# Kernel tuning notes

Measured on AMD Instinct MI355X. Metric: run time of the kernel, lower is better.

Reference implementation:

```python
import jax, jax.numpy as jnp
import numpy as np

B, M, L = 100, 100, 8
N = M * L
EPS = 1e-5  # torch BatchNorm2d default eps


def _conv(x, w, b, stride, pad):
    y = jax.lax.conv_general_dilated(x, w, (stride, stride), [(pad, pad), (pad, pad)],
                                     dimension_numbers=('NCHW', 'OIHW', 'NCHW'))
    return y + b[None, :, None, None]


def _convT(x, w, b, stride, pad):
    # torch ConvTranspose2d weight layout: (in_ch, out_ch, kH, kW)
    k = w.shape[2]
    wt = jnp.flip(w, (2, 3)).transpose(1, 0, 2, 3)  # -> OIHW
    p = k - 1 - pad
    y = jax.lax.conv_general_dilated(x, wt, (1, 1), [(p, p), (p, p)],
                                     lhs_dilation=(stride, stride),
                                     dimension_numbers=('NCHW', 'OIHW', 'NCHW'))
    return y + b[None, :, None, None]


def _bn(x):
    # BatchNorm2d constructed fresh in forward: weight=1, bias=0, batch stats (biased var)
    mean = x.mean(axis=(0, 2, 3), keepdims=True)
    var = x.var(axis=(0, 2, 3), keepdims=True)
    return (x - mean) / jnp.sqrt(var + EPS)


def _leaky(x):
    return jnp.where(x >= 0, x, 0.01 * x)


def _forward(x, conv1_w, conv1_b, conv2_w, conv2_b, conv3_w, conv3_b, conv4_w, conv4_b,
             fc_w, fc_b, dec_w, dec_b, ct1_w, ct1_b, ct2_w, ct2_b, ct3_w, ct3_b,
             ct4_w, ct4_b, ct5_w, ct5_b):
    # ---- encoder ----
    h = _bn(_leaky(_conv(x, conv1_w, conv1_b, 2, 1)))   # (B,128,32,32)
    h = _bn(_leaky(_conv(h, conv2_w, conv2_b, 2, 1)))   # (B,256,16,16)
    h = _bn(_leaky(_conv(h, conv3_w, conv3_b, 2, 1)))   # (B,1024,8,8)
    h = _bn(_leaky(_conv(h, conv4_w, conv4_b, 2, 1)))   # (B,1024,4,4)
    eig = jax.nn.relu(h.reshape(B, -1) @ fc_w + fc_b)   # (B, 800)
    # ---- latent_sample (training branch) ----
    sig = eig.reshape(B, M, L)
    row = jnp.sqrt(float(M * L)) * jnp.fft.ifft2(sig)          # complex (B,M,L)
    # original builds C via numpy/scipy per-sample -> detached; circulant[i,j] = c[(i-j) % n]
    row_flat = jax.lax.stop_gradient(row.real.reshape(B, N))
    i = jnp.arange(N)
    idx = (i[:, None] - i[None, :]) % N                        # (N,N) circulant gather
    C = row_flat[:, idx]                                       # (B,N,N)
    # original: Sigma_batch_eps[:, i] = eigenvalue (noise zeta is dead code), via numpy -> detached
    Y = jnp.fft.fft2(jax.lax.stop_gradient(sig)).real          # (B,M,L)
    # ---- decoder ----
    d = (Y.reshape(B, N) @ dec_w + dec_b).reshape(B, 1024, 3, 3)
    d = _convT(d, ct1_w, ct1_b, 2, 1)   # (B,512,5,5)
    d = _convT(d, ct2_w, ct2_b, 2, 0)   # (B,256,11,11)
    d = _convT(d, ct3_w, ct3_b, 2, 0)   # (B,128,23,23)
    d = _convT(d, ct4_w, ct4_b, 2, 0)   # (B,64,47,47)
    d = _convT(d, ct5_w, ct5_b, 1, 0)   # (B,1,49,49)
    return d, C, eig


def setup_inputs():
    key = jax.random.key(0)
    ks = jax.random.split(key, 16)

    def wv(k, shape, fan_in):
        return (jax.random.normal(k, shape, jnp.float32) / np.sqrt(fan_in)).astype(jnp.float32)

    return {
        'x': jax.random.normal(ks[0], (B, 1, 64, 64), jnp.float32),
        'conv1_w': wv(ks[1], (128, 1, 3, 3), 9), 'conv1_b': jnp.zeros((128,), jnp.float32),
        'conv2_w': wv(ks[2], (256, 128, 3, 3), 128 * 9), 'conv2_b': jnp.zeros((256,), jnp.float32),
        'conv3_w': wv(ks[3], (1024, 256, 3, 3), 256 * 9), 'conv3_b': jnp.zeros((1024,), jnp.float32),
        'conv4_w': wv(ks[4], (1024, 1024, 3, 3), 1024 * 9), 'conv4_b': jnp.zeros((1024,), jnp.float32),
        'fc_w': wv(ks[5], (1024 * 16, N), 1024 * 16), 'fc_b': jnp.zeros((N,), jnp.float32),
        'dec_w': wv(ks[6], (N, 1024 * 9), N), 'dec_b': jnp.zeros((1024 * 9,), jnp.float32),
        'ct1_w': wv(ks[7], (1024, 512, 3, 3), 1024 * 9), 'ct1_b': jnp.zeros((512,), jnp.float32),
        'ct2_w': wv(ks[8], (512, 256, 3, 3), 512 * 9), 'ct2_b': jnp.zeros((256,), jnp.float32),
        'ct3_w': wv(ks[9], (256, 128, 3, 3), 256 * 9), 'ct3_b': jnp.zeros((128,), jnp.float32),
        'ct4_w': wv(ks[10], (128, 64, 3, 3), 128 * 9), 'ct4_b': jnp.zeros((64,), jnp.float32),
        'ct5_w': wv(ks[11], (64, 1, 3, 3), 64 * 9), 'ct5_b': jnp.zeros((1,), jnp.float32),
    }


def reference(x, conv1_w, conv1_b, conv2_w, conv2_b, conv3_w, conv3_b, conv4_w, conv4_b,
              fc_w, fc_b, dec_w, dec_b, ct1_w, ct1_b, ct2_w, ct2_b, ct3_w, ct3_b,
              ct4_w, ct4_b, ct5_w, ct5_b):
    return _forward(x, conv1_w, conv1_b, conv2_w, conv2_b, conv3_w, conv3_b, conv4_w, conv4_b,
                    fc_w, fc_b, dec_w, dec_b, ct1_w, ct1_b, ct2_w, ct2_b, ct3_w, ct3_b,
                    ct4_w, ct4_b, ct5_w, ct5_b)
```

## Files before the change

### kernel.cpp

```cpp
#include <hip/hip_runtime.h>
#include <math.h>

typedef __attribute__((ext_vector_type(8))) short bf16x8;
typedef __attribute__((ext_vector_type(4))) float f32x4;
typedef unsigned short u16;

__device__ __forceinline__ u16 f2bf(float f) {
    unsigned u = __builtin_bit_cast(unsigned, f);
    u += 0x7FFFu + ((u >> 16) & 1u);
    return (u16)(u >> 16);
}
__device__ __forceinline__ float bf2f(u16 h) {
    unsigned u = ((unsigned)h) << 16;
    return __builtin_bit_cast(float, u);
}

template<int MODE, int OUT, int BM, int BN, int SWIZ, bool STATS>
__global__ __launch_bounds__(256, 3)
void gemm(const u16* __restrict__ Abf, const u16* __restrict__ Bw,
          const float* __restrict__ bias, void* __restrict__ outv,
          float* __restrict__ stat,
          int M, int N, int K, int lgC,
          int IH, int IW, int OH, int OW, int zchunk)
{
    constexpr int ANSEG = BM / 64, BNSEG = BN / 64;
    constexpr int RM = BM / 32, RN = BN / 32;
    __shared__ __align__(16) u16 As[2][4 * BM * 8];
    __shared__ __align__(16) u16 Bs[2][4 * BN * 8];
    const int t = threadIdx.x;
    const int lane = t & 63, wave = t >> 6;
    const int lm = lane & 15, quad = lane >> 4;
    const int wm = wave & 1, wn = wave >> 1;
    int mt, nt, z;
    if (SWIZ == 1) {
        int mtN = (M + BM - 1) / BM;
        int id = blockIdx.x;
        nt = id & 7; int j = id >> 3;
        mt = j % mtN; z = j / mtN;
    } else { mt = blockIdx.x; nt = blockIdx.y; z = blockIdx.z; }
    const int k0 = z * zchunk, kend = k0 + zchunk;

    const int arow = (ANSEG == 2) ? (t >> 1) : (t >> 2);
    const int akb  = (ANSEG == 2) ? (t & 1) * 16 : (t & 3) * 8;
    const int a_gm = mt * BM + arow;
    const bool a_in = a_gm < M;
    int oy = 0, ox = 0, bimg = 0;
    if (MODE == 1) {
        int ohw = OH * OW;
        int g = a_in ? a_gm : 0;
        bimg = g / ohw; int r = g - bimg * ohw;
        oy = r / OW; ox = r - (r / OW) * OW;
    }
    const int brow = (BNSEG == 2) ? (t >> 1) : (t >> 2);
    const int bkb  = (BNSEG == 2) ? (t & 1) * 16 : (t & 3) * 8;
    const int b_gn = nt * BN + brow;
    const bool b_in = b_gn < N;

    const int Cmask = (1 << lgC) - 1;
    int ic_s = 0, tap_s = 0;
    bool aok = a_in;
    const u16* aptr;
    if (MODE == 0) {
        aptr = Abf + (size_t)a_gm * K + k0 + akb;
    } else {
        int kk0 = k0 + akb;
        tap_s = kk0 >> lgC; ic_s = kk0 & Cmask;
        int ky = tap_s / 3, kx = tap_s - (tap_s / 3) * 3;
        int iy = oy * 2 - 1 + ky, ix = ox * 2 - 1 + kx;
        aok = a_in && (unsigned)iy < (unsigned)IH && (unsigned)ix < (unsigned)IW;
        aptr = Abf + ((((size_t)bimg * IH + iy) * IW + ix) << lgC);
    }
    const u16* bptr = Bw + (size_t)b_gn * K + k0 + bkb;

    auto ldA = [&](uint4 (&v)[ANSEG]) {
        #pragma unroll
        for (int s = 0; s < ANSEG; s++) {
            uint4 x4 = make_uint4(0, 0, 0, 0);
            if (MODE == 0) {
                if (aok) x4 = *(const uint4*)(aptr + s * 8);
            } else {
                if (aok) x4 = *(const uint4*)(aptr + ic_s + s * 8);
            }
            v[s] = x4;
        }
        if (MODE == 0) {
            aptr += 32;
        } else {
            ic_s += 32;
            if (ic_s > Cmask) {
                ic_s -= Cmask + 1;
                tap_s++;
                int ky = tap_s / 3, kx = tap_s - (tap_s / 3) * 3;
                int iy = oy * 2 - 1 + ky, ix = ox * 2 - 1 + kx;
                aok = a_in && (unsigned)iy < (unsigned)IH && (unsigned)ix < (unsigned)IW;
                aptr = Abf + ((((size_t)bimg * IH + iy) * IW + ix) << lgC);
            }
        }
    };
    auto ldB = [&](uint4 (&v)[BNSEG]) {
        #pragma unroll
        for (int s = 0; s < BNSEG; s++) {
            uint4 x4 = make_uint4(0, 0, 0, 0);
            if (b_in) x4 = *(const uint4*)(bptr + s * 8);
            v[s] = x4;
        }
        bptr += 32;
    };

    f32x4 acc[RM][RN];
    #pragma unroll
    for (int i = 0; i < RM; i++)
        #pragma unroll
        for (int j = 0; j < RN; j++) acc[i][j] = (f32x4){0.f, 0.f, 0.f, 0.f};

    uint4 va[ANSEG], vb[BNSEG];
    ldA(va); ldB(vb);
    int buf = 0;
    for (int kb = k0; kb < kend; kb += 32) {
        #pragma unroll
        for (int s = 0; s < ANSEG; s++)
            *(uint4*)&As[buf][(((akb >> 3) + s) * BM + arow) * 8] = va[s];
        #pragma unroll
        for (int s = 0; s < BNSEG; s++)
            *(uint4*)&Bs[buf][(((bkb >> 3) + s) * BN + brow) * 8] = vb[s];
        __syncthreads();
        if (kb + 32 < kend) { ldA(va); ldB(vb); }
        bf16x8 af[RM], bfr[RN];
        #pragma unroll
        for (int i = 0; i < RM; i++)
            af[i] = *(const bf16x8*)&As[buf][(size_t)(quad * BM + wm * (BM / 2) + i * 16 + lm) * 8];
        #pragma unroll
        for (int j = 0; j < RN; j++)
            bfr[j] = *(const bf16x8*)&Bs[buf][(size_t)(quad * BN + wn * (BN / 2) + j * 16 + lm) * 8];
        #pragma unroll
        for (int i = 0; i < RM; i++)
            #pragma unroll
            for (int j = 0; j < RN; j++)
                acc[i][j] = __builtin_amdgcn_mfma_f32_16x16x32_bf16(af[i], bfr[j], acc[i][j], 0, 0, 0);
        buf ^= 1;
    }

    const int n_base = nt * BN + wn * (BN / 2);
    const int m_base = mt * BM + wm * (BM / 2);
    int nj[RN]; float bvj[RN];
    #pragma unroll
    for (int j = 0; j < RN; j++) {
        nj[j] = n_base + j * 16 + lm;
        bvj[j] = 0.f;
        if (nj[j] < N && OUT != 4) {
            if (OUT == 0) bvj[j] = bias[nj[j]];
            else if (OUT == 6) bvj[j] = bias[(nj[j] & 1023) * 9 + (nj[j] >> 10)];
            else if (z == 0) bvj[j] = bias[nj[j]];
        }
    }
    if constexpr (OUT == 4) {
        float* op = (float*)outv;
        #pragma unroll
        for (int i = 0; i < RM; i++)
            #pragma unroll
            for (int r = 0; r < 4; r++) {
                int m = m_base + i * 16 + quad * 4 + r;
                if (m >= M) continue;
                #pragma unroll
                for (int j = 0; j < RN; j++)
                    if (nj[j] < N) atomicAdd(&op[(size_t)m * N + nj[j]], acc[i][j][r]);
            }
    } else if constexpr (OUT == 6) {
        u16* op = (u16*)outv;
        #pragma unroll
        for (int i = 0; i < RM; i++)
            #pragma unroll
            for (int r = 0; r < 4; r++) {
                int m = m_base + i * 16 + quad * 4 + r;
                if (m >= M) continue;
                #pragma unroll
                for (int j = 0; j < RN; j++)
                    if (nj[j] < N) op[(size_t)m * N + nj[j]] = f2bf(acc[i][j][r] + bvj[j]);
            }
    } else if constexpr (OUT == 0) {
        int ohw = OH * OW;
        float sj[RN], qj[RN];
        #pragma unroll
        for (int j = 0; j < RN; j++) { sj[j] = 0.f; qj[j] = 0.f; }
        #pragma unroll
        for (int i = 0; i < RM; i++) {
            int m0 = m_base + i * 16 + quad * 4;
            if (m0 >= M) continue;
            int b = m0 / ohw, pix = m0 - b * ohw;
            #pragma unroll
            for (int j = 0; j < RN; j++) {
                if (nj[j] >= N) continue;
                #pragma unroll
                for (int r = 0; r < 4; r++) {
                    float val = acc[i][j][r] + bvj[j];
                    ((u16*)outv)[((size_t)b * ohw + pix + r) * N + nj[j]] = f2bf(val);
                    if (STATS) {
                        float lv = val >= 0.f ? val : 0.01f * val;
                        sj[j] += lv; qj[j] += lv * lv;
                    }
                }
            }
        }
        if constexpr (STATS) {
            #pragma unroll
            for (int j = 0; j < RN; j++) {
                float s = sj[j], q = qj[j];
                s += __shfl_down(s, 32); q += __shfl_down(q, 32);
                s += __shfl_down(s, 16); q += __shfl_down(q, 16);
                if (quad == 0 && nj[j] < N) {
                    atomicAdd(&stat[nj[j]], s);
                    atomicAdd(&stat[N + nj[j]], q);
                }
            }
        }
    } else {
        int ohw = OH * OW;
        #pragma unroll
        for (int i = 0; i < RM; i++) {
            int m0 = m_base + i * 16 + quad * 4;
            if (m0 >= M) continue;
            int b = m0 / ohw, pix = m0 - b * ohw;
            #pragma unroll
            for (int j = 0; j < RN; j++) {
                if (nj[j] >= N) continue;
                #pragma unroll
                for (int r = 0; r < 4; r++)
                    atomicAdd(&((float*)outv)[((size_t)b * ohw + pix + r) * N + nj[j]],
                              acc[i][j][r] + bvj[j]);
            }
        }
    }
}

template<int BM>
__global__ __launch_bounds__(256, 3)
void gemm_ct(const u16* __restrict__ Abf, const u16* __restrict__ Wb,
             const float* __restrict__ bias, u16* __restrict__ out,
             int N, int lgC, int IH, int IW, int OH, int OW,
             int4 Kc, int4 Mc, int4 Hc, int4 Wc, int4 Oc, int4 Dy, int4 Dx)
{
    constexpr int ANSEG = BM / 64;
    constexpr int RM = BM / 32, RN = 2;
    const int c = blockIdx.z;
    const int Ks[4] = {Kc.x, Kc.y, Kc.z, Kc.w};
    const int Ms[4] = {Mc.x, Mc.y, Mc.z, Mc.w};
    const int Hs[4] = {Hc.x, Hc.y, Hc.z, Hc.w};
    const int Wsz[4]= {Wc.x, Wc.y, Wc.z, Wc.w};
    const int Os[4] = {Oc.x, Oc.y, Oc.z, Oc.w};
    const int Dys[4]= {Dy.x, Dy.y, Dy.z, Dy.w};
    const int Dxs[4]= {Dx.x, Dx.y, Dx.z, Dx.w};
    const int K = Ks[c], M = Ms[c], OHc = Hs[c], OWc = Wsz[c];
    const int dyp = Dys[c], dxp = Dxs[c];
    const int mt = blockIdx.x, nt = blockIdx.y;
    if (mt * BM >= M) return;
    const u16* Bw = Wb + Os[c];

    __shared__ __align__(16) u16 As[2][4 * BM * 8];
    __shared__ __align__(16) u16 Bs[2][4 * 64 * 8];
    const int t = threadIdx.x;
    const int lane = t & 63, wave = t >> 6;
    const int lm = lane & 15, quad = lane >> 4;
    const int wm = wave & 1, wn = wave >> 1;

    const int arow = (ANSEG == 2) ? (t >> 1) : (t >> 2);
    const int akb  = (ANSEG == 2) ? (t & 1) * 16 : (t & 3) * 8;
    const int a_gm = mt * BM + arow;
    const bool a_in = a_gm < M;
    const int ohwc = OHc * OWc;
    int g = a_in ? a_gm : 0;
    int bimg = g / ohwc; int rr = g - bimg * ohwc;
    int oy = rr / OWc, ox = rr - (rr / OWc) * OWc;

    const int brow = t >> 2;
    const int bkb  = (t & 3) * 8;
    const int b_gn = nt * 64 + brow;
    const bool b_in = b_gn < N;

    const int Cmask = (1 << lgC) - 1;
    int ic_s = akb & Cmask;
    int ti_s = 0;
    bool aok; const u16* aptr;
    {
        int sh = 8 * (ti_s & 3);
        int dy = (int)(signed char)((dyp >> sh) & 255);
        int dx = (int)(signed char)((dxp >> sh) & 255);
        int iy = oy + dy, ix = ox + dx;
        aok = a_in && (unsigned)iy < (unsigned)IH && (unsigned)ix < (unsigned)IW;
        aptr = Abf + ((((size_t)bimg * IH + iy) * IW + ix) << lgC);
    }
    const u16* bptr = Bw + (size_t)b_gn * K + bkb;

    auto ldA = [&](uint4 (&v)[ANSEG]) {
        #pragma unroll
        for (int s = 0; s < ANSEG; s++) {
            uint4 x4 = make_uint4(0, 0, 0, 0);
            if (aok) x4 = *(const uint4*)(aptr + ic_s + s * 8);
            v[s] = x4;
        }
        ic_s += 32;
        if (ic_s > Cmask) {
            ic_s -= Cmask + 1;
            ti_s++;
            int sh = 8 * (ti_s & 3);
            int dy = (int)(signed char)((dyp >> sh) & 255);
            int dx = (int)(signed char)((dxp >> sh) & 255);
            int iy = oy + dy, ix = ox + dx;
            aok = a_in && (unsigned)iy < (unsigned)IH && (unsigned)ix < (unsigned)IW;
            aptr = Abf + ((((size_t)bimg * IH + iy) * IW + ix) << lgC);
        }
    };
    auto ldB = [&](uint4& v) {
        uint4 x4 = make_uint4(0, 0, 0, 0);
        if (b_in) x4 = *(const uint4*)bptr;
        v = x4;
        bptr += 32;
    };

    f32x4 acc[RM][RN];
    #pragma unroll
    for (int i = 0; i < RM; i++)
        #pragma unroll
        for (int j = 0; j < RN; j++) acc[i][j] = (f32x4){0.f, 0.f, 0.f, 0.f};

    uint4 va[ANSEG]; uint4 vb;
    ldA(va); ldB(vb);
    int buf = 0;
    for (int kb = 0; kb < K; kb += 32) {
        #pragma unroll
        for (int s = 0; s < ANSEG; s++)
            *(uint4*)&As[buf][(((akb >> 3) + s) * BM + arow) * 8] = va[s];
        *(uint4*)&Bs[buf][((bkb >> 3) * 64 + brow) * 8] = vb;
        __syncthreads();
        if (kb + 32 < K) { ldA(va); ldB(vb); }
        bf16x8 af[RM], bfr[RN];
        #pragma unroll
        for (int i = 0; i < RM; i++)
            af[i] = *(const bf16x8*)&As[buf][(size_t)(quad * BM + wm * (BM / 2) + i * 16 + lm) * 8];
        #pragma unroll
        for (int j = 0; j < RN; j++)
            bfr[j] = *(const bf16x8*)&Bs[buf][(size_t)(quad * 64 + wn * 32 + j * 16 + lm) * 8];
        #pragma unroll
        for (int i = 0; i < RM; i++)
            #pragma unroll
            for (int j = 0; j < RN; j++)
                acc[i][j] = __builtin_amdgcn_mfma_f32_16x16x32_bf16(af[i], bfr[j], acc[i][j], 0, 0, 0);
        buf ^= 1;
    }

    const int n_base = nt * 64 + wn * 32;
    const int m_base = mt * BM + wm * (BM / 2);
    const int cy = c >> 1, cx = c & 1;
    const int OHW = OH * OW;
    int nj[RN]; float bvj[RN];
    #pragma unroll
    for (int j = 0; j < RN; j++) {
        nj[j] = n_base + j * 16 + lm;
        bvj[j] = (nj[j] < N) ? bias[nj[j]] : 0.f;
    }
    #pragma unroll
    for (int i = 0; i < RM; i++)
        #pragma unroll
        for (int r = 0; r < 4; r++) {
            int m = m_base + i * 16 + quad * 4 + r;
            if (m >= M) continue;
            int b = m / ohwc, r2 = m - b * ohwc;
            int oyc = r2 / OWc, oxc = r2 - (r2 / OWc) * OWc;
            size_t ad0 = ((size_t)b * OHW + (2 * oyc + cy) * OW + 2 * oxc + cx) * N;
            #pragma unroll
            for (int j = 0; j < RN; j++)
                if (nj[j] < N) out[ad0 + nj[j]] = f2bf(acc[i][j][r] + bvj[j]);
        }
}

__global__ __launch_bounds__(256)
void convw_prep(const float* __restrict__ src, u16* __restrict__ dst, int lgC) {
    __shared__ float tl[9216];
    int CIN = 1 << lgC;
    int n = CIN * 9;
    size_t base = (size_t)blockIdx.x * n;
    for (int i = threadIdx.x; i < n; i += 256) tl[i] = src[base + i];
    __syncthreads();
    for (int j = threadIdx.x; j < n; j += 256) {
        int tap = j >> lgC, ic = j & (CIN - 1);
        dst[base + j] = f2bf(tl[ic * 9 + tap]);
    }
}

__global__ __launch_bounds__(256)
void transpose_cvt_dec(const float* __restrict__ in, u16* __restrict__ out) {
    __shared__ float tl[32][33];
    int c0 = blockIdx.x * 32, r0 = blockIdx.y * 32;
    int tx = threadIdx.x & 31, ty = threadIdx.x >> 5;
    #pragma unroll
    for (int l = 0; l < 4; l++)
        tl[ty + 8 * l][tx] = in[(size_t)(r0 + ty + 8 * l) * 9216 + c0 + tx];
    __syncthreads();
    #pragma unroll
    for (int l = 0; l < 4; l++) {
        int n = c0 + ty + 8 * l;
        int cc = n / 9, hw = n - 9 * cc;
        out[(size_t)(hw * 1024 + cc) * 800 + r0 + tx] = f2bf(tl[tx][ty + 8 * l]);
    }
}

__global__ __launch_bounds__(256)
void ctw_fused(const float* __restrict__ in, u16* __restrict__ outw,
               int CIN, int P, int4 Kc, int4 Oc) {
    __shared__ float tl[32][33];
    int c0 = blockIdx.x * 32, r0 = blockIdx.y * 32;
    int C = gridDim.x * 32;
    int tx = threadIdx.x & 31, ty = threadIdx.x >> 5;
    #pragma unroll
    for (int l = 0; l < 4; l++)
        tl[ty + 8 * l][tx] = in[(size_t)(r0 + ty + 8 * l) * C + c0 + tx];
    __syncthreads();
    const int Ks[4] = {Kc.x, Kc.y, Kc.z, Kc.w};
    const int Os[4] = {Oc.x, Oc.y, Oc.z, Oc.w};
    int ic = r0 + tx;
    #pragma unroll
    for (int l = 0; l < 4; l++) {
        int cc = c0 + ty + 8 * l;
        int oc = cc / 9, tap = cc - 9 * oc;
        int ky = tap / 3, kx = tap - 3 * (tap / 3);
        int cyc = (P + ky) & 1, cxc = (P + kx) & 1;
        int cls = cyc * 2 + cxc;
        int nkx = ((P ^ cxc) & 1) ? 1 : 2;
        int ti = (ky >> 1) * nkx + (kx >> 1);
        outw[Os[cls] + (size_t)oc * Ks[cls] + ti * CIN + ic] = f2bf(tl[tx][ty + 8 * l]);
    }
}

__global__ __launch_bounds__(256)
void fcw_prep(const float* __restrict__ in, u16* __restrict__ out) {
    __shared__ float tl[32][33];
    int n0 = blockIdx.x * 32, c0 = blockIdx.y * 32, hw = blockIdx.z;
    int tx = threadIdx.x & 31, ty = threadIdx.x >> 5;
    #pragma unroll
    for (int l = 0; l < 4; l++)
        tl[ty + 8 * l][tx] = in[((size_t)(c0 + ty + 8 * l) * 16 + hw) * 800 + n0 + tx];
    __syncthreads();
    #pragma unroll
    for (int l = 0; l < 4; l++)
        out[(size_t)(n0 + ty + 8 * l) * 16384 + hw * 1024 + c0 + tx] = f2bf(tl[tx][ty + 8 * l]);
}

__global__ __launch_bounds__(256)
void wt5_prep(const float* __restrict__ in, u16* __restrict__ out) {
    int idx = blockIdx.x * 256 + threadIdx.x;
    if (idx >= 576) return;
    int tap = idx >> 6, ic = idx & 63;
    out[idx] = f2bf(in[ic * 9 + tap]);
}

__global__ __launch_bounds__(256)
void conv1_stat(const float* __restrict__ x, const float* __restrict__ w,
                const float* __restrict__ bias, u16* __restrict__ out,
                float* __restrict__ accum) {
    __shared__ float ls[256];
    ls[threadIdx.x] = 0.f;
    __syncthreads();
    int idx0 = blockIdx.x * 256 + threadIdx.x;
    int oc = idx0 & 127;
    float wreg[9];
    const float* wp = w + oc * 9;
    #pragma unroll
    for (int k = 0; k < 9; k++) wreg[k] = wp[k];
    float bz = bias[oc];
    float s = 0.f, q = 0.f;
    for (int idx = idx0; idx < 13107200; idx += 262144) {
        int pix = (idx >> 7) & 1023;
        int b = idx >> 17;
        int oy = pix >> 5, ox = pix & 31;
        int iy0 = oy * 2 - 1, ix0 = ox * 2 - 1;
        float acc = bz;
        const float* ip = x + (size_t)b * 4096;
        #pragma unroll
        for (int ky = 0; ky < 3; ky++) {
            int iy = iy0 + ky;
            if ((unsigned)iy >= 64u) continue;
            #pragma unroll
            for (int kx = 0; kx < 3; kx++) {
                int ix = ix0 + kx;
                if ((unsigned)ix >= 64u) continue;
                acc = fmaf(ip[iy * 64 + ix], wreg[ky * 3 + kx], acc);
            }
        }
        out[idx] = f2bf(acc);
        float lv = acc >= 0.f ? acc : 0.01f * acc;
        s += lv; q += lv * lv;
    }
    atomicAdd(&ls[oc], s);
    atomicAdd(&ls[128 + oc], q);
    __syncthreads();
    atomicAdd(&accum[threadIdx.x], ls[threadIdx.x]);
}

__global__ __launch_bounds__(256)
void bnapply8(const u16* __restrict__ x, u16* __restrict__ out,
              const float* __restrict__ accum, int C, int total, float invcnt) {
    int i8 = (blockIdx.x * 256 + threadIdx.x) * 8;
    if (i8 >= total) return;
    int c0 = i8 & (C - 1);
    uint4 v = *(const uint4*)(x + i8);
    const unsigned* w = (const unsigned*)&v;
    uint4 o;
    unsigned* ow = (unsigned*)&o;
    #pragma unroll
    for (int h = 0; h < 4; h++) {
        float m0 = accum[c0 + 2 * h] * invcnt, m1 = accum[c0 + 2 * h + 1] * invcnt;
        float q0 = accum[C + c0 + 2 * h] * invcnt, q1 = accum[C + c0 + 2 * h + 1] * invcnt;
        float in0 = rsqrtf(q0 - m0 * m0 + 1e-5f);
        float in1 = rsqrtf(q1 - m1 * m1 + 1e-5f);
        float v0 = __builtin_bit_cast(float, w[h] << 16);
        float v1 = __builtin_bit_cast(float, w[h] & 0xFFFF0000u);
        v0 = v0 >= 0.f ? v0 : 0.01f * v0;
        v1 = v1 >= 0.f ? v1 : 0.01f * v1;
        unsigned r0 = f2bf((v0 - m0) * in0);
        unsigned r1 = f2bf((v1 - m1) * in1);
        ow[h] = r0 | (r1 << 16);
    }
    *(uint4*)(out + i8) = o;
}

__global__ __launch_bounds__(256)
void bnstat4f(const float* __restrict__ x, float* __restrict__ accum, int C, int total) {
    __shared__ float ls[2048];
    for (int i = threadIdx.x; i < 2 * C; i += 256) ls[i] = 0.f;
    __syncthreads();
    int base = (blockIdx.x * 256 + threadIdx.x) * 4;
    int stride = gridDim.x * 1024;
    float s[4] = {0, 0, 0, 0}, q[4] = {0, 0, 0, 0};
    for (int i = base; i < total; i += stride) {
        f32x4 v = *(const f32x4*)(x + i);
        #pragma unroll
        for (int r = 0; r < 4; r++) {
            float vv = v[r]; vv = vv >= 0.f ? vv : 0.01f * vv;
            s[r] += vv; q[r] += vv * vv;
        }
    }
    int c0 = base & (C - 1);
    #pragma unroll
    for (int r = 0; r < 4; r++) {
        atomicAdd(&ls[c0 + r], s[r]);
        atomicAdd(&ls[C + c0 + r], q[r]);
    }
    __syncthreads();
    for (int i = threadIdx.x; i < 2 * C; i += 256) atomicAdd(&accum[i], ls[i]);
}

__global__ __launch_bounds__(256)
void bnapply4f(const float* __restrict__ x, u16* __restrict__ out,
               const float* __restrict__ accum, int C, int total, float invcnt) {
    int i4 = (blockIdx.x * 256 + threadIdx.x) * 4;
    if (i4 >= total) return;
    int c0 = i4 & (C - 1);
    f32x4 v = *(const f32x4*)(x + i4);
    unsigned r4[4];
    #pragma unroll
    for (int r = 0; r < 4; r++) {
        float m = accum[c0 + r] * invcnt;
        float var = accum[C + c0 + r] * invcnt - m * m;
        float inv = rsqrtf(var + 1e-5f);
        float vv = v[r]; vv = vv >= 0.f ? vv : 0.01f * vv;
        r4[r] = f2bf((vv - m) * inv);
    }
    *(uint2*)(out + i4) = make_uint2(r4[0] | (r4[1] << 16), r4[2] | (r4[3] << 16));
}

__global__ __launch_bounds__(256)
void dft_real(const float* __restrict__ facc, const float* __restrict__ fcb,
              float* __restrict__ eig, float* __restrict__ Yr, u16* __restrict__ Yrb) {
    __shared__ float se[800];
    __shared__ float ctab[800];
    int b = blockIdx.x;
    for (int i = threadIdx.x; i < 800; i += 256) {
        float v = fmaxf(facc[b * 800 + i] + fcb[i], 0.f);
        se[i] = v;
        if (blockIdx.y == 0) eig[b * 800 + i] = v;
        ctab[i] = cospif(i * 0.0025f);
    }
    __syncthreads();
    int o0 = blockIdx.y * 400;
    for (int oi = o0 + threadIdx.x; oi < o0 + 400; oi += 256) {
        int k1 = oi >> 3, k2 = oi & 7;
        int d1 = k1 * 8, d2 = k2 * 100;
        float acc0 = 0.f, acc1 = 0.f;
        int p1 = 0;
        for (int n1 = 0; n1 < 100; n1 += 2) {
            int p = p1;
            #pragma unroll
            for (int n2 = 0; n2 < 8; n2++) {
                acc0 = fmaf(se[n1 * 8 + n2], ctab[p], acc0);
                p += d2; if (p >= 800) p -= 800;
            }
            int pb = p1 + d1; if (pb >= 800) pb -= 800;
            int p2 = pb;
            #pragma unroll
            for (int n2 = 0; n2 < 8; n2++) {
                acc1 = fmaf(se[(n1 + 1) * 8 + n2], ctab[p2], acc1);
                p2 += d2; if (p2 >= 800) p2 -= 800;
            }
            p1 = pb + d1; if (p1 >= 800) p1 -= 800;
        }
        float acc = acc0 + acc1;
        Yr[b * 800 + oi] = acc;
        Yrb[b * 800 + oi] = f2bf(acc);
    }
}

__global__ __launch_bounds__(256)
void build_C4(const float* __restrict__ Yr, float* __restrict__ C) {
    int idx = blockIdx.x * 256 + threadIdx.x;
    if (idx >= 100 * 800 * 200) return;
    int j4 = (idx % 200) * 4; int tt = idx / 200;
    int i = tt % 800;         int b = tt / 800;
    const float* y = Yr + b * 800;
    f32x4 v;
    #pragma unroll
    for (int r = 0; r < 4; r++) {
        int k = i - (j4 + r);
        k += (k >> 31) & 800;
        v[r] = y[k] * 0.035355339059327376f;
    }
    ((f32x4*)C)[idx] = v;
}

__global__ __launch_bounds__(256)
void convT5(const u16* __restrict__ in, const u16* __restrict__ w,
            const float* __restrict__ bias, float* __restrict__ out) {
    int idx = blockIdx.x * 256 + threadIdx.x;
    if (idx >= 100 * 49 * 49) return;
    int ox = idx % 49; int t2 = idx / 49;
    int oy = t2 % 49;  int b = t2 / 49;
    float ac[8];
    #pragma unroll
    for (int r = 0; r < 8; r++) ac[r] = 0.f;
    for (int ky = 0; ky < 3; ky++) {
        int iy = oy - ky;
        if ((unsigned)iy >= 47u) continue;
        for (int kx = 0; kx < 3; kx++) {
            int ix = ox - kx;
            if ((unsigned)ix >= 47u) continue;
            const uint4* ip = (const uint4*)(in + (((size_t)b * 47 + iy) * 47 + ix) * 64);
            const uint4* wp = (const uint4*)(w + (ky * 3 + kx) * 64);
            #pragma unroll
            for (int g = 0; g < 8; g++) {
                uint4 av = ip[g], wv = wp[g];
                const unsigned* aa = (const unsigned*)&av;
                const unsigned* ww = (const unsigned*)&wv;
                #pragma unroll
                for (int h = 0; h < 4; h++) {
                    float a0 = __builtin_bit_cast(float, aa[h] << 16);
                    float a1 = __builtin_bit_cast(float, aa[h] & 0xFFFF0000u);
                    float w0 = __builtin_bit_cast(float, ww[h] << 16);
                    float w1 = __builtin_bit_cast(float, ww[h] & 0xFFFF0000u);
                    int rix = ((g & 1) << 2) | h;
                    ac[rix] = fmaf(a0, w0, ac[rix]);
                    ac[rix] = fmaf(a1, w1, ac[rix]);
                }
            }
        }
    }
    out[idx] = bias[0] + ((ac[0] + ac[1]) + (ac[2] + ac[3]))
                       + ((ac[4] + ac[5]) + (ac[6] + ac[7]));
}

struct CTClass { int T, OHc, OWc, dyp, dxp, off, K; };
static void ct_params(int P, int OH, int OW, int CIN, int OC, CTClass cls[4]) {
    int off = 0;
    for (int c = 0; c < 4; c++) {
        int cy = c >> 1, cx = c & 1;
        int kys[2], dys[2], nky = 0, kxs[2], dxs[2], nkx = 0;
        for (int ky = 0; ky < 3; ky++)
            if (((cy + P + ky) & 1) == 0) { kys[nky] = ky; dys[nky] = (cy + P - ky) / 2; nky++; }
        for (int kx = 0; kx < 3; kx++)
            if (((cx + P + kx) & 1) == 0) { kxs[nkx] = kx; dxs[nkx] = (cx + P - kx) / 2; nkx++; }
        CTClass& cc = cls[c];
        cc.T = nky * nkx;
        cc.OHc = (OH - cy + 1) >> 1; cc.OWc = (OW - cx + 1) >> 1;
        cc.dyp = 0; cc.dxp = 0;
        int ti = 0;
        for (int a = 0; a < nky; a++)
            for (int b2 = 0; b2 < nkx; b2++, ti++) {
                cc.dyp |= (dys[a] & 255) << (8 * ti);
                cc.dxp |= (dxs[b2] & 255) << (8 * ti);
            }
        cc.off = off; cc.K = CIN * cc.T;
        off += OC * cc.K;
    }
}

template<int BM>
static void launch_ct(hipStream_t s, const u16* in, const u16* W, const float* bias, u16* outp,
                      int lgC, int OC, int IH, int IW, int OH, int OW, const CTClass* cls) {
    int maxMT = 0;
    for (int c = 0; c < 4; c++) {
        int mt = (100 * cls[c].OHc * cls[c].OWc + BM - 1) / BM;
        if (mt > maxMT) maxMT = mt;
    }
    dim3 g(maxMT, (OC + 63) / 64, 4);
    gemm_ct<BM><<<g, 256, 0, s>>>(in, W, bias, outp, OC, lgC, IH, IW, OH, OW,
        make_int4(cls[0].K, cls[1].K, cls[2].K, cls[3].K),
        make_int4(100*cls[0].OHc*cls[0].OWc, 100*cls[1].OHc*cls[1].OWc,
                  100*cls[2].OHc*cls[2].OWc, 100*cls[3].OHc*cls[3].OWc),
        make_int4(cls[0].OHc, cls[1].OHc, cls[2].OHc, cls[3].OHc),
        make_int4(cls[0].OWc, cls[1].OWc, cls[2].OWc, cls[3].OWc),
        make_int4(cls[0].off, cls[1].off, cls[2].off, cls[3].off),
        make_int4(cls[0].dyp, cls[1].dyp, cls[2].dyp, cls[3].dyp),
        make_int4(cls[0].dxp, cls[1].dxp, cls[2].dxp, cls[3].dxp));
}

static void launch_ctw(hipStream_t s, const float* w, u16* outw,
                       int CIN, int OC, int P, const CTClass* cls) {
    dim3 g((OC * 9) / 32, CIN / 32);
    ctw_fused<<<g, 256, 0, s>>>(w, outw, CIN, P,
        make_int4(cls[0].K, cls[1].K, cls[2].K, cls[3].K),
        make_int4(cls[0].off, cls[1].off, cls[2].off, cls[3].off));
}

extern "C" void kernel_launch(void* const* d_in, const int* in_sizes, int n_in,
                              void* d_out, int out_size, void* d_ws, size_t ws_size,
                              hipStream_t stream) {
    const float* x    = (const float*)d_in[0];
    const float* c1w  = (const float*)d_in[1];  const float* c1b = (const float*)d_in[2];
    const float* c2w  = (const float*)d_in[3];  const float* c2b = (const float*)d_in[4];
    const float* c3w  = (const float*)d_in[5];  const float* c3b = (const float*)d_in[6];
    const float* c4w  = (const float*)d_in[7];  const float* c4b = (const float*)d_in[8];
    const float* fcw  = (const float*)d_in[9];  const float* fcb = (const float*)d_in[10];
    const float* decw = (const float*)d_in[11]; const float* decb = (const float*)d_in[12];
    const float* t1w  = (const float*)d_in[13]; const float* t1b = (const float*)d_in[14];
    const float* t2w  = (const float*)d_in[15]; const float* t2b = (const float*)d_in[16];
    const float* t3w  = (const float*)d_in[17]; const float* t3b = (const float*)d_in[18];
    const float* t4w  = (const float*)d_in[19]; const float* t4b = (const float*)d_in[20];
    const float* t5w  = (const float*)d_in[21]; const float* t5b = (const float*)d_in[22];

    float* out = (float*)d_out;
    float* d_final = out;
    float* Cmat    = out + 240100;
    float* eig     = out + 240100 + 64000000;

    float* ws = (float*)d_ws;
    u16*   h1    = (u16*)(ws);
    u16*   W_fc  = (u16*)(ws);
    u16*   h2    = (u16*)(ws + 6553600);
    u16*   h3    = (u16*)(ws + 9830400);
    u16*   W_c2  = (u16*)(ws + 13107200);
    u16*   W_c3  = (u16*)(ws + 13254656);
    u16*   W_c4  = (u16*)(ws + 14434304);
    float* h4f   = ws + 19152896;
    u16*   h4    = (u16*)(ws + 20791296);
    float* accs  = ws + 21610496;
    float* facc  = ws + 21618688;
    float* Yr    = ws + 21698688;
    u16*   Yrb   = (u16*)(ws + 21778688);
    u16*   d0    = (u16*)(ws + 21818688);
    u16*   W_dec = (u16*)(ws + 22279488);
    float* acc1 = accs, *acc2 = accs + 2048, *acc3 = accs + 4096, *acc4 = accs + 6144;
    u16*   W_t   = (u16*)(ws);
    u16*   o1    = (u16*)(ws + 4718592);
    u16*   o2    = (u16*)(ws + 5358592);
    u16*   o3    = (u16*)(ws + 6907392);
    u16*   o4    = (u16*)(ws + 10292992);
    u16*   W_t5  = (u16*)(ws + 17361792);

    #define GRID(n) dim3(((n) + 255) / 256)

    hipMemsetAsync(accs, 0, (8192 + 80000) * 4, stream);

    conv1_stat<<<dim3(1024), 256, 0, stream>>>(x, c1w, c1b, h1, acc1);
    bnapply8<<<GRID(1638400), 256, 0, stream>>>(h1, h1, acc1, 128, 13107200, 1.f / 102400.f);

    convw_prep<<<dim3(256), 256, 0, stream>>>(c2w, W_c2, 7);
    gemm<1, 0, 128, 128, 0, true><<<dim3(200, 2, 1), 256, 0, stream>>>(
        h1, W_c2, c2b, h2, acc2, 25600, 256, 1152, 7, 32, 32, 16, 16, 1152);
    bnapply8<<<GRID(819200), 256, 0, stream>>>(h2, h2, acc2, 256, 6553600, 1.f / 25600.f);

    convw_prep<<<dim3(1024), 256, 0, stream>>>(c3w, W_c3, 8);
    gemm<1, 0, 128, 128, 1, true><<<dim3(400, 1, 1), 256, 0, stream>>>(
        h2, W_c3, c3b, h3, acc3, 6400, 1024, 2304, 8, 16, 16, 8, 8, 2304);
    bnapply8<<<GRID(819200), 256, 0, stream>>>(h3, h3, acc3, 1024, 6553600, 1.f / 6400.f);

    convw_prep<<<dim3(1024), 256, 0, stream>>>(c4w, W_c4, 10);
    hipMemsetAsync(h4f, 0, 1638400 * 4, stream);
    gemm<1, 1, 64, 128, 1, false><<<dim3(400, 1, 1), 256, 0, stream>>>(
        h3, W_c4, c4b, h4f, nullptr, 1600, 1024, 9216, 10, 8, 8, 4, 4, 4608);
    bnstat4f<<<1024, 256, 0, stream>>>(h4f, acc4, 1024, 1638400);
    bnapply4f<<<GRID(409600), 256, 0, stream>>>(h4f, h4, acc4, 1024, 1638400, 1.f / 1600.f);

    fcw_prep<<<dim3(25, 32, 16), 256, 0, stream>>>(fcw, W_fc);
    gemm<0, 4, 64, 64, 0, false><<<dim3(2, 13, 16), 256, 0, stream>>>(
        h4, W_fc, nullptr, facc, nullptr, 100, 800, 16384, 0, 0, 0, 0, 0, 1024);

    dft_real<<<dim3(100, 2), 256, 0, stream>>>(facc, fcb, eig, Yr, Yrb);
    build_C4<<<GRID(16000000), 256, 0, stream>>>(Yr, Cmat);

    transpose_cvt_dec<<<dim3(288, 25), 256, 0, stream>>>(decw, W_dec);
    gemm<0, 6, 64, 64, 0, false><<<dim3(2, 144, 1), 256, 0, stream>>>(
        Yrb, W_dec, decb, d0, nullptr, 100, 9216, 800, 0, 0, 0, 0, 0, 800);

    CTClass c1c[4], c2c[4], c3c[4], c4c[4];
    ct_params(1, 5, 5, 1024, 512, c1c);
    ct_params(0, 11, 11, 512, 256, c2c);
    ct_params(0, 23, 23, 256, 128, c3c);
    ct_params(0, 47, 47, 128, 64, c4c);

    launch_ctw(stream, t1w, W_t, 1024, 512, 1, c1c);
    launch_ct<64>(stream, d0, W_t, t1b, o1, 10, 512, 3, 3, 5, 5, c1c);

    launch_ctw(stream, t2w, W_t, 512, 256, 0, c2c);
    launch_ct<64>(stream, o1, W_t, t2b, o2, 9, 256, 5, 5, 11, 11, c2c);

    launch_ctw(stream, t3w, W_t, 256, 128, 0, c3c);
    launch_ct<64>(stream, o2, W_t, t3b, o3, 8, 128, 11, 11, 23, 23, c3c);

    launch_ctw(stream, t4w, W_t, 128, 64, 0, c4c);
    launch_ct<128>(stream, o3, W_t, t4b, o4, 7, 64, 23, 23, 47, 47, c4c);

    wt5_prep<<<GRID(576), 256, 0, stream>>>(t5w, W_t5);
    convT5<<<GRID(240100), 256, 0, stream>>>(o4, W_t5, t5b, d_final);

    #undef GRID
}
```

Baseline: 1.080 ms.

## Merge all weight-prep kernels into one launch and shrink encoder GEMM tiles

All per-layer weight conversion and transpose kernels are folded into a single prep_all kernel, launched once up front. Each weight now gets its own workspace region instead of reusing aliased buffers, which removes about ten launches and their serialization. The conv2/conv3 GEMMs also move from 128x128 to 64x128 tiles with twice the blocks, and conv4's split-K chunk is halved to double its grid. The cost is a larger workspace footprint, a heavy block-dispatch branch, and the 36KB shared array in prep_all, which may limit occupancy for the small transpose tasks.

```diff
diff --git a/kernel.cpp b/kernel.cpp
--- a/kernel.cpp
+++ b/kernel.cpp
@@ -372,12 +372,13 @@
         }
 }
 
-__global__ __launch_bounds__(256)
-void convw_prep(const float* __restrict__ src, u16* __restrict__ dst, int lgC) {
-    __shared__ float tl[9216];
+
+__device__ __forceinline__ void convw_task(const float* __restrict__ src,
+                                           u16* __restrict__ dst, int lgC,
+                                           int bx, float* tl) {
     int CIN = 1 << lgC;
     int n = CIN * 9;
-    size_t base = (size_t)blockIdx.x * n;
+    size_t base = (size_t)bx * n;
     for (int i = threadIdx.x; i < n; i += 256) tl[i] = src[base + i];
     __syncthreads();
     for (int j = threadIdx.x; j < n; j += 256) {
@@ -386,10 +387,24 @@
     }
 }
 
-__global__ __launch_bounds__(256)
-void transpose_cvt_dec(const float* __restrict__ in, u16* __restrict__ out) {
-    __shared__ float tl[32][33];
-    int c0 = blockIdx.x * 32, r0 = blockIdx.y * 32;
+__device__ __forceinline__ void fcw_task(const float* __restrict__ in,
+                                         u16* __restrict__ out,
+                                         int bx, int by, int bz, float (*tl)[33]) {
+    int n0 = bx * 32, c0 = by * 32, hw = bz;
+    int tx = threadIdx.x & 31, ty = threadIdx.x >> 5;
+    #pragma unroll
+    for (int l = 0; l < 4; l++)
+        tl[ty + 8 * l][tx] = in[((size_t)(c0 + ty + 8 * l) * 16 + hw) * 800 + n0 + tx];
+    __syncthreads();
+    #pragma unroll
+    for (int l = 0; l < 4; l++)
+        out[(size_t)(n0 + ty + 8 * l) * 16384 + hw * 1024 + c0 + tx] = f2bf(tl[tx][ty + 8 * l]);
+}
+
+__device__ __forceinline__ void dec_task(const float* __restrict__ in,
+                                         u16* __restrict__ out,
+                                         int bx, int by, float (*tl)[33]) {
+    int c0 = bx * 32, r0 = by * 32;
     int tx = threadIdx.x & 31, ty = threadIdx.x >> 5;
     #pragma unroll
     for (int l = 0; l < 4; l++)
@@ -403,12 +418,12 @@
     }
 }
 
-__global__ __launch_bounds__(256)
-void ctw_fused(const float* __restrict__ in, u16* __restrict__ outw,
-               int CIN, int P, int4 Kc, int4 Oc) {
-    __shared__ float tl[32][33];
-    int c0 = blockIdx.x * 32, r0 = blockIdx.y * 32;
-    int C = gridDim.x * 32;
+__device__ __forceinline__ void ctw_task(const float* __restrict__ in,
+                                         u16* __restrict__ outw,
+                                         int CIN, int P, int4 Kc, int4 Oc,
+                                         int bx, int by, int nbx, float (*tl)[33]) {
+    int c0 = bx * 32, r0 = by * 32;
+    int C = nbx * 32;
     int tx = threadIdx.x & 31, ty = threadIdx.x >> 5;
     #pragma unroll
     for (int l = 0; l < 4; l++)
@@ -431,25 +446,45 @@
 }
 
 __global__ __launch_bounds__(256)
-void fcw_prep(const float* __restrict__ in, u16* __restrict__ out) {
-    __shared__ float tl[32][33];
-    int n0 = blockIdx.x * 32, c0 = blockIdx.y * 32, hw = blockIdx.z;
-    int tx = threadIdx.x & 31, ty = threadIdx.x >> 5;
-    #pragma unroll
-    for (int l = 0; l < 4; l++)
-        tl[ty + 8 * l][tx] = in[((size_t)(c0 + ty + 8 * l) * 16 + hw) * 800 + n0 + tx];
-    __syncthreads();
-    #pragma unroll
-    for (int l = 0; l < 4; l++)
-        out[(size_t)(n0 + ty + 8 * l) * 16384 + hw * 1024 + c0 + tx] = f2bf(tl[tx][ty + 8 * l]);
-}
-
-__global__ __launch_bounds__(256)
-void wt5_prep(const float* __restrict__ in, u16* __restrict__ out) {
-    int idx = blockIdx.x * 256 + threadIdx.x;
-    if (idx >= 576) return;
-    int tap = idx >> 6, ic = idx & 63;
-    out[idx] = f2bf(in[ic * 9 + tap]);
+void prep_all(const float* __restrict__ c2w, u16* __restrict__ W_c2,
+              const float* __restrict__ c3w, u16* __restrict__ W_c3,
+              const float* __restrict__ c4w, u16* __restrict__ W_c4,
+              const float* __restrict__ fcw, u16* __restrict__ W_fc,
+              const float* __restrict__ decw, u16* __restrict__ W_dec,
+              const float* __restrict__ t1w, u16* __restrict__ Wt1, int4 K1, int4 O1,
+              const float* __restrict__ t2w, u16* __restrict__ Wt2, int4 K2, int4 O2,
+              const float* __restrict__ t3w, u16* __restrict__ Wt3, int4 K3, int4 O3,
+              const float* __restrict__ t4w, u16* __restrict__ Wt4, int4 K4, int4 O4,
+              const float* __restrict__ t5w, u16* __restrict__ Wt5)
+{
+    __shared__ float tl[9216];
+    float (*t2)[33] = (float(*)[33])tl;
+    int b = blockIdx.x;
+    if (b < 256)               { convw_task(c2w, W_c2, 7,  b, tl); return; }
+    b -= 256;
+    if (b < 1024)              { convw_task(c3w, W_c3, 8,  b, tl); return; }
+    b -= 1024;
+    if (b < 1024)              { convw_task(c4w, W_c4, 10, b, tl); return; }
+    b -= 1024;
+    if (b < 12800)             { fcw_task(fcw, W_fc, b % 25, (b / 25) % 32, b / 800, t2); return; }
+    b -= 12800;
+    if (b < 7200)              { dec_task(decw, W_dec, b % 288, b / 288, t2); return; }
+    b -= 7200;
+    if (b < 4608)              { ctw_task(t1w, Wt1, 1024, 1, K1, O1, b % 144, b / 144, 144, t2); return; }
+    b -= 4608;
+    if (b < 1152)              { ctw_task(t2w, Wt2, 512, 0, K2, O2, b % 72, b / 72, 72, t2); return; }
+    b -= 1152;
+    if (b < 288)               { ctw_task(t3w, Wt3, 256, 0, K3, O3, b % 36, b / 36, 36, t2); return; }
+    b -= 288;
+    if (b < 72)                { ctw_task(t4w, Wt4, 128, 0, K4, O4, b % 18, b / 18, 18, t2); return; }
+    b -= 72;
+    {
+        int idx = b * 256 + threadIdx.x;
+        if (idx < 576) {
+            int tap = idx >> 6, ic = idx & 63;
+            Wt5[idx] = f2bf(t5w[ic * 9 + tap]);
+        }
+    }
 }
 
 __global__ __launch_bounds__(256)
@@ -689,6 +724,8 @@
         off += OC * cc.K;
     }
 }
+static int4 cK(const CTClass* c) { return make_int4(c[0].K, c[1].K, c[2].K, c[3].K); }
+static int4 cO(const CTClass* c) { return make_int4(c[0].off, c[1].off, c[2].off, c[3].off); }
 
 template<int BM>
 static void launch_ct(hipStream_t s, const u16* in, const u16* W, const float* bias, u16* outp,
@@ -700,22 +737,14 @@
     }
     dim3 g(maxMT, (OC + 63) / 64, 4);
     gemm_ct<BM><<<g, 256, 0, s>>>(in, W, bias, outp, OC, lgC, IH, IW, OH, OW,
-        make_int4(cls[0].K, cls[1].K, cls[2].K, cls[3].K),
+        cK(cls),
         make_int4(100*cls[0].OHc*cls[0].OWc, 100*cls[1].OHc*cls[1].OWc,
                   100*cls[2].OHc*cls[2].OWc, 100*cls[3].OHc*cls[3].OWc),
         make_int4(cls[0].OHc, cls[1].OHc, cls[2].OHc, cls[3].OHc),
         make_int4(cls[0].OWc, cls[1].OWc, cls[2].OWc, cls[3].OWc),
-        make_int4(cls[0].off, cls[1].off, cls[2].off, cls[3].off),
+        cO(cls),
         make_int4(cls[0].dyp, cls[1].dyp, cls[2].dyp, cls[3].dyp),
         make_int4(cls[0].dxp, cls[1].dxp, cls[2].dxp, cls[3].dxp));
-}
-
-static void launch_ctw(hipStream_t s, const float* w, u16* outw,
-                       int CIN, int OC, int P, const CTClass* cls) {
-    dim3 g((OC * 9) / 32, CIN / 32);
-    ctw_fused<<<g, 256, 0, s>>>(w, outw, CIN, P,
-        make_int4(cls[0].K, cls[1].K, cls[2].K, cls[3].K),
-        make_int4(cls[0].off, cls[1].off, cls[2].off, cls[3].off));
 }
 
 extern "C" void kernel_launch(void* const* d_in, const int* in_sizes, int n_in,
@@ -741,7 +770,6 @@
 
     float* ws = (float*)d_ws;
     u16*   h1    = (u16*)(ws);
-    u16*   W_fc  = (u16*)(ws);
     u16*   h2    = (u16*)(ws + 6553600);
     u16*   h3    = (u16*)(ws + 9830400);
     u16*   W_c2  = (u16*)(ws + 13107200);
@@ -756,47 +784,16 @@
     u16*   d0    = (u16*)(ws + 21818688);
     u16*   W_dec = (u16*)(ws + 22279488);
     float* acc1 = accs, *acc2 = accs + 2048, *acc3 = accs + 4096, *acc4 = accs + 6144;
-    u16*   W_t   = (u16*)(ws);
+    u16*   W_fc  = (u16*)(ws + 25965888);
+    u16*   Wt1   = (u16*)(ws + 32519488);
+    u16*   Wt2   = (u16*)(ws + 34878784);
+    u16*   Wt3   = (u16*)(ws + 35468608);
+    u16*   Wt4   = (u16*)(ws + 35616064);
+    u16*   Wt5   = (u16*)(ws + 35652928);
     u16*   o1    = (u16*)(ws + 4718592);
     u16*   o2    = (u16*)(ws + 5358592);
     u16*   o3    = (u16*)(ws + 6907392);
     u16*   o4    = (u16*)(ws + 10292992);
-    u16*   W_t5  = (u16*)(ws + 17361792);
-
-    #define GRID(n) dim3(((n) + 255) / 256)
-
-    hipMemsetAsync(accs, 0, (8192 + 80000) * 4, stream);
-
-    conv1_stat<<<dim3(1024), 256, 0, stream>>>(x, c1w, c1b, h1, acc1);
-    bnapply8<<<GRID(1638400), 256, 0, stream>>>(h1, h1, acc1, 128, 13107200, 1.f / 102400.f);
-
-    convw_prep<<<dim3(256), 256, 0, stream>>>(c2w, W_c2, 7);
-    gemm<1, 0, 128, 128, 0, true><<<dim3(200, 2, 1), 256, 0, stream>>>(
-        h1, W_c2, c2b, h2, acc2, 25600, 256, 1152, 7, 32, 32, 16, 16, 1152);
-    bnapply8<<<GRID(819200), 256, 0, stream>>>(h2, h2, acc2, 256, 6553600, 1.f / 25600.f);
-
-    convw_prep<<<dim3(1024), 256, 0, stream>>>(c3w, W_c3, 8);
-    gemm<1, 0, 128, 128, 1, true><<<dim3(400, 1, 1), 256, 0, stream>>>(
-        h2, W_c3, c3b, h3, acc3, 6400, 1024, 2304, 8, 16, 16, 8, 8, 2304);
-    bnapply8<<<GRID(819200), 256, 0, stream>>>(h3, h3, acc3, 1024, 6553600, 1.f / 6400.f);
-
-    convw_prep<<<dim3(1024), 256, 0, stream>>>(c4w, W_c4, 10);
-    hipMemsetAsync(h4f, 0, 1638400 * 4, stream);
-    gemm<1, 1, 64, 128, 1, false><<<dim3(400, 1, 1), 256, 0, stream>>>(
-        h3, W_c4, c4b, h4f, nullptr, 1600, 1024, 9216, 10, 8, 8, 4, 4, 4608);
-    bnstat4f<<<1024, 256, 0, stream>>>(h4f, acc4, 1024, 1638400);
-    bnapply4f<<<GRID(409600), 256, 0, stream>>>(h4f, h4, acc4, 1024, 1638400, 1.f / 1600.f);
-
-    fcw_prep<<<dim3(25, 32, 16), 256, 0, stream>>>(fcw, W_fc);
-    gemm<0, 4, 64, 64, 0, false><<<dim3(2, 13, 16), 256, 0, stream>>>(
-        h4, W_fc, nullptr, facc, nullptr, 100, 800, 16384, 0, 0, 0, 0, 0, 1024);
-
-    dft_real<<<dim3(100, 2), 256, 0, stream>>>(facc, fcb, eig, Yr, Yrb);
-    build_C4<<<GRID(16000000), 256, 0, stream>>>(Yr, Cmat);
-
-    transpose_cvt_dec<<<dim3(288, 25), 256, 0, stream>>>(decw, W_dec);
-    gemm<0, 6, 64, 64, 0, false><<<dim3(2, 144, 1), 256, 0, stream>>>(
-        Yrb, W_dec, decb, d0, nullptr, 100, 9216, 800, 0, 0, 0, 0, 0, 800);
 
     CTClass c1c[4], c2c[4], c3c[4], c4c[4];
     ct_params(1, 5, 5, 1024, 512, c1c);
@@ -804,20 +801,50 @@
     ct_params(0, 23, 23, 256, 128, c3c);
     ct_params(0, 47, 47, 128, 64, c4c);
 
-    launch_ctw(stream, t1w, W_t, 1024, 512, 1, c1c);
-    launch_ct<64>(stream, d0, W_t, t1b, o1, 10, 512, 3, 3, 5, 5, c1c);
-
-    launch_ctw(stream, t2w, W_t, 512, 256, 0, c2c);
-    launch_ct<64>(stream, o1, W_t, t2b, o2, 9, 256, 5, 5, 11, 11, c2c);
-
-    launch_ctw(stream, t3w, W_t, 256, 128, 0, c3c);
-    launch_ct<64>(stream, o2, W_t, t3b, o3, 8, 128, 11, 11, 23, 23, c3c);
-
-    launch_ctw(stream, t4w, W_t, 128, 64, 0, c4c);
-    launch_ct<128>(stream, o3, W_t, t4b, o4, 7, 64, 23, 23, 47, 47, c4c);
-
-    wt5_prep<<<GRID(576), 256, 0, stream>>>(t5w, W_t5);
-    convT5<<<GRID(240100), 256, 0, stream>>>(o4, W_t5, t5b, d_final);
+    #define GRID(n) dim3(((n) + 255) / 256)
+
+    hipMemsetAsync(accs, 0, (8192 + 80000) * 4, stream);
+
+    prep_all<<<dim3(28427), 256, 0, stream>>>(
+        c2w, W_c2, c3w, W_c3, c4w, W_c4, fcw, W_fc, decw, W_dec,
+        t1w, Wt1, cK(c1c), cO(c1c),
+        t2w, Wt2, cK(c2c), cO(c2c),
+        t3w, Wt3, cK(c3c), cO(c3c),
+        t4w, Wt4, cK(c4c), cO(c4c),
+        t5w, Wt5);
+
+    conv1_stat<<<dim3(1024), 256, 0, stream>>>(x, c1w, c1b, h1, acc1);
+    bnapply8<<<GRID(1638400), 256, 0, stream>>>(h1, h1, acc1, 128, 13107200, 1.f / 102400.f);
+
+    gemm<1, 0, 64, 128, 0, true><<<dim3(400, 2, 1), 256, 0, stream>>>(
+        h1, W_c2, c2b, h2, acc2, 25600, 256, 1152, 7, 32, 32, 16, 16, 1152);
+    bnapply8<<<GRID(819200), 256, 0, stream>>>(h2, h2, acc2, 256, 6553600, 1.f / 25600.f);
+
+    gemm<1, 0, 64, 128, 1, true><<<dim3(800, 1, 1), 256, 0, stream>>>(
+        h2, W_c3, c3b, h3, acc3, 6400, 1024, 2304, 8, 16, 16, 8, 8, 2304);
+    bnapply8<<<GRID(819200), 256, 0, stream>>>(h3, h3, acc3, 1024, 6553600, 1.f / 6400.f);
+
+    hipMemsetAsync(h4f, 0, 1638400 * 4, stream);
+    gemm<1, 1, 64, 128, 1, false><<<dim3(800, 1, 1), 256, 0, stream>>>(
+        h3, W_c4, c4b, h4f, nullptr, 1600, 1024, 9216, 10, 8, 8, 4, 4, 2304);
+    bnstat4f<<<1024, 256, 0, stream>>>(h4f, acc4, 1024, 1638400);
+    bnapply4f<<<GRID(409600), 256, 0, stream>>>(h4f, h4, acc4, 1024, 1638400, 1.f / 1600.f);
+
+    gemm<0, 4, 64, 64, 0, false><<<dim3(2, 13, 16), 256, 0, stream>>>(
+        h4, W_fc, nullptr, facc, nullptr, 100, 800, 16384, 0, 0, 0, 0, 0, 1024);
+
+    dft_real<<<dim3(100, 2), 256, 0, stream>>>(facc, fcb, eig, Yr, Yrb);
+    build_C4<<<GRID(16000000), 256, 0, stream>>>(Yr, Cmat);
+
+    gemm<0, 6, 64, 64, 0, false><<<dim3(2, 144, 1), 256, 0, stream>>>(
+        Yrb, W_dec, decb, d0, nullptr, 100, 9216, 800, 0, 0, 0, 0, 0, 800);
+
+    launch_ct<64>(stream, d0, Wt1, t1b, o1, 10, 512, 3, 3, 5, 5, c1c);
+    launch_ct<64>(stream, o1, Wt2, t2b, o2, 9, 256, 5, 5, 11, 11, c2c);
+    launch_ct<64>(stream, o2, Wt3, t3b, o3, 8, 128, 11, 11, 23, 23, c3c);
+    launch_ct<128>(stream, o3, Wt4, t4b, o4, 7, 64, 23, 23, 47, 47, c4c);
+
+    convT5<<<GRID(240100), 256, 0, stream>>>(o4, Wt5, t5b, d_final);
 
     #undef GRID
 }
```

Result: slower. 1.109 ms (+2.6%).
